# Kernel tuning notes

Measured on AMD Instinct MI355X. Metric: run time of the kernel, lower is better.

The kernel has to match this reference:

```python
import jax, jax.numpy as jnp
import numpy as np
import math
from jax.scipy.special import gammaln

B, H, W = 32, 960, 960
BLOCK = 96  # official NIQE/NRQM block size

# AGGD shape-parameter lookup table (same grid as torch impl: 0.2..10 step 0.001)
_GAM_NP = np.arange(0.2, 10.0 + 1e-6, 0.001, dtype=np.float64)
_RG_NP = np.array([math.exp(2.0 * math.lgamma(2.0 / g) - math.lgamma(1.0 / g) - math.lgamma(3.0 / g)) for g in _GAM_NP], dtype=np.float32)
GAM = jnp.asarray(_GAM_NP.astype(np.float32))
RGAM = jnp.asarray(_RG_NP)

def _gauss_kernel(size, sigma):
    ax = np.arange(size, dtype=np.float64) - (size - 1) / 2.0
    xx, yy = np.meshgrid(ax, ax)
    k = np.exp(-(xx ** 2 + yy ** 2) / (2.0 * sigma ** 2))
    return (k / k.sum()).astype(np.float32)

K7 = jnp.asarray(_gauss_kernel(7, 7.0 / 6.0))[None, None]  # MSCN window
K3 = jnp.asarray(_gauss_kernel(3, 0.5))[None, None]        # pyramid / downsample kernel

def _conv_same(x, k, edge_pad):
    ph = k.shape[-1] // 2
    mode = 'edge' if edge_pad else 'constant'
    x = jnp.pad(x, ((0, 0), (0, 0), (ph, ph), (ph, ph)), mode=mode)
    return jax.lax.conv_general_dilated(x, k, (1, 1), 'VALID', dimension_numbers=('NCHW', 'OIHW', 'NCHW'))

def _normalize(img):
    # MSCN: (img - mu) / (sigma + 1), replicate padding
    mu = _conv_same(img, K7, True)
    sigma = jnp.sqrt(jnp.abs(_conv_same(img * img, K7, True) - mu * mu))
    return (img - mu) / (sigma + 1.0)

def _downsample(img):
    # gaussian blur (3x3, sigma 0.5, zero same-pad) + stride-2 decimation
    return _conv_same(img, K3, False)[:, :, ::2, ::2]

def _aggd(x):
    # x: [b, nb, h, w]; vectorized AGGD parameter estimation over all blocks
    hw = (-2, -1)
    x2 = x * x
    ml = (x < 0).astype(x.dtype)
    mr = (x > 0).astype(x.dtype)
    cl = jnp.maximum(ml.sum(hw), 1.0)
    cr = jnp.maximum(mr.sum(hw), 1.0)
    lstd = jnp.sqrt((x2 * ml).sum(hw) / cl)
    rstd = jnp.sqrt((x2 * mr).sum(hw) / cr)
    gh = lstd / jnp.maximum(rstd, 1e-12)
    rhat = jnp.mean(jnp.abs(x), hw) ** 2 / jnp.maximum(jnp.mean(x2, hw), 1e-12)
    rhn = rhat * (gh ** 3 + 1.0) * (gh + 1.0) / ((gh * gh + 1.0) ** 2)
    idx = jnp.argmin(jnp.abs(RGAM - rhn[..., None]), axis=-1)  # table lookup
    alpha = GAM[idx]
    conv = jnp.exp(0.5 * (gammaln(1.0 / alpha) - gammaln(3.0 / alpha)))
    return alpha, lstd * conv, rstd * conv

def _features(blocks):
    # 18 features per block: AGGD of block + AGGD of 4 shifted products
    alpha, bl, br = _aggd(blocks)
    feats = [alpha, (bl + br) / 2.0]
    for shift in ((0, 1), (1, 0), (1, 1), (1, -1)):
        sb = jnp.roll(blocks, shift, axis=(2, 3))
        a, l, r = _aggd(blocks * sb)
        mean = (r - l) * jnp.exp(gammaln(2.0 / a) - gammaln(1.0 / a))
        feats += [a, mean, l, r]
    return jnp.stack(feats, axis=-1)  # [b, nb, 18]

def _blocks(x, bs):
    b, _, h, w = x.shape
    nh, nw = h // bs, w // bs
    x = x[:, 0].reshape(b, nh, bs, nw, bs).transpose(0, 1, 3, 2, 4)
    return x.reshape(b, nh * nw, bs, bs)

def setup_inputs() -> dict:
    key = jax.random.key(0)
    k1, k2, k3 = jax.random.split(key, 3)
    X = jax.random.uniform(k1, (B, 1, H, W), jnp.float32) * 255.0
    mu_pris = jax.random.normal(k2, (36,), jnp.float32)
    A = jax.random.normal(k3, (36, 36), jnp.float32)
    cov_pris = A @ A.T / 36.0 + jnp.eye(36, dtype=jnp.float32)  # SPD pristine covariance
    return {"X": X, "mu_pris": mu_pris, "cov_pris": cov_pris}

def reference(X, mu_pris, cov_pris):
    feats = []
    img = X
    for scale in (1, 2):
        xn = _normalize(img)
        feats.append(_features(_blocks(xn, BLOCK // scale)))  # [b, 100, 18]
        if scale == 1:
            img = _downsample(img)
    d = jnp.concatenate(feats, axis=-1)  # [b, nb, 36]
    mu_dist = d.mean(axis=1)  # [b, 36]
    c = d - mu_dist[:, None, :]
    cov_dist = jnp.einsum('bnf,bng->bfg', c, c) / (d.shape[1] - 1)
    invcov = jnp.linalg.pinv((cov_pris[None] + cov_dist) / 2.0)
    diff = mu_pris[None] - mu_dist
    q = jnp.einsum('bf,bfg,bg->b', diff, invcov, diff)
    return jnp.sqrt(jnp.maximum(q, 0.0))
```

## Files before the change

### kernel.cpp

```cpp
#include <hip/hip_runtime.h>
#include <hip/hip_fp16.h>
#include <math.h>

#define NTAB 9801
typedef unsigned int uint;
typedef float f2v __attribute__((ext_vector_type(2)));
typedef _Float16 h2v __attribute__((ext_vector_type(2)));

struct WParams { float w1[7]; float wd[3]; };

__device__ inline __half2 u2h2(uint u) { return __builtin_bit_cast(__half2, u); }
__device__ inline float flo(uint u) { return __low2float(u2h2(u)); }
__device__ inline float fhi(uint u) { return __high2float(u2h2(u)); }
__device__ inline uint pkmul(uint a, uint b) { return __builtin_bit_cast(uint, __hmul2(u2h2(a), u2h2(b))); }
__device__ inline uint pack2(float a, float b) {
    return __builtin_bit_cast(uint, __builtin_amdgcn_cvt_pkrtz(a, b));
}
__device__ inline uint algn16(uint hi, uint lo) {
    return (uint)((((unsigned long long)hi << 32) | lo) >> 16);
}
__device__ inline float fdot2f(uint a, uint b, float c) {
    return __builtin_amdgcn_fdot2(__builtin_bit_cast(h2v, a), __builtin_bit_cast(h2v, b), c, false);
}
__device__ inline float rcpf(float x) { return __builtin_amdgcn_rcpf(x); }

template <int S, bool FUSE_DOWN, typename TIN>
__device__ __forceinline__ void mscn_body(int bid, uint* tin,
                                          const TIN* __restrict__ src,
                                          uint* __restrict__ xn_out,
                                          __half* __restrict__ down_out,
                                          const WParams& wp) {
    constexpr int ROW_W = 132, H_OUT = 28, H_IN = H_OUT + 6, RPT = H_OUT / 2;
    constexpr int NTX = (S + 255) / 256, NTY = (S + H_OUT - 1) / H_OUT;

    const int tid = threadIdx.x;
    const int b  = bid / (NTX * NTY);
    const int t2 = bid % (NTX * NTY);
    const int x0 = min((t2 / NTY) * 256, S - 256);
    const int y0 = min((t2 % NTY) * H_OUT, S - H_OUT);

    const float* w1 = wp.w1;
    uint wA[4], wB[4];
    wA[0] = pack2(0.f, w1[0]);   wA[1] = pack2(w1[1], w1[2]);
    wA[2] = pack2(w1[3], w1[4]); wA[3] = pack2(w1[5], w1[6]);
    wB[0] = pack2(w1[0], w1[1]); wB[1] = pack2(w1[2], w1[3]);
    wB[2] = pack2(w1[4], w1[5]); wB[3] = pack2(w1[6], 0.f);

    const TIN* img = src + (size_t)b * S * S;
    const bool interior = (x0 >= 4) && (x0 <= S - 260) && (y0 >= 3) && (y0 <= S - H_IN + 3);

    if constexpr (sizeof(TIN) == 4) {
        if (interior) {
            const float4* base = reinterpret_cast<const float4*>(
                (const float*)img + (size_t)(y0 - 3) * S + (x0 - 4));
            const int f4row = S / 4;
            for (int i = tid; i < 66 * H_IN; i += 256) {
                int r = i / 66, k = i - r * 66;
                float4 v = base[(size_t)r * f4row + k];
                uint2 pr; pr.x = pack2(v.x, v.y); pr.y = pack2(v.z, v.w);
                *(uint2*)&tin[r * ROW_W + 2 * k] = pr;
            }
        } else {
            for (int i = tid; i < ROW_W * H_IN; i += 256) {
                int r = i / ROW_W, w = i - r * ROW_W;
                int gy = y0 + r - 3; gy = gy < 0 ? 0 : (gy >= S ? S - 1 : gy);
                int c0 = x0 - 4 + 2 * w; int c0c = c0 < 0 ? 0 : (c0 >= S ? S - 1 : c0);
                int c1 = c0 + 1;         int c1c = c1 < 0 ? 0 : (c1 >= S ? S - 1 : c1);
                const TIN* rp = img + (size_t)gy * S;
                tin[i] = pack2((float)rp[c0c], (float)rp[c1c]);
            }
        }
    } else {
        const uint* gw = (const uint*)img;
        for (int i = tid; i < ROW_W * H_IN; i += 256) {
            int r = i / ROW_W, w = i - r * ROW_W;
            int gy = y0 + r - 3; gy = gy < 0 ? 0 : (gy >= S ? S - 1 : gy);
            int c0 = x0 - 4 + 2 * w;
            if (c0 >= 0 && c0 + 1 < S) {
                tin[i] = gw[((size_t)gy * S + c0) >> 1];
            } else {
                int c0c = c0 < 0 ? 0 : (c0 >= S ? S - 1 : c0);
                int c1c = (c0 + 1) < 0 ? 0 : ((c0 + 1) >= S ? S - 1 : c0 + 1);
                const TIN* rp = img + (size_t)gy * S;
                tin[i] = pack2((float)rp[c0c], (float)rp[c1c]);
            }
        }
    }
    __syncthreads();

    const int g = tid >> 7, c = tid & 127;
    const int R0 = g * RPT;

    auto horiz = [&](int row, f2v& o1, f2v& o2) {
        const uint* pw = &tin[row * ROW_W + c];
        uint q0 = pw[0], q1 = pw[1], q2 = pw[2], q3 = pw[3], q4 = pw[4];
        uint p0 = pkmul(q0, q0), p1 = pkmul(q1, q1), p2 = pkmul(q2, q2),
             p3 = pkmul(q3, q3), p4 = pkmul(q4, q4);
        float s1A = fdot2f(q3, wA[3], fdot2f(q2, wA[2], fdot2f(q1, wA[1], fdot2f(q0, wA[0], 0.f))));
        float s2A = fdot2f(p3, wA[3], fdot2f(p2, wA[2], fdot2f(p1, wA[1], fdot2f(p0, wA[0], 0.f))));
        float s1B = fdot2f(q4, wB[3], fdot2f(q3, wB[2], fdot2f(q2, wB[1], fdot2f(q1, wB[0], 0.f))));
        float s2B = fdot2f(p4, wB[3], fdot2f(p3, wB[2], fdot2f(p2, wB[1], fdot2f(p1, wB[0], 0.f))));
        o1 = (f2v){s1A, s1B};
        o2 = (f2v){s2A, s2B};
    };

    f2v r1[7], r2[7];
#pragma unroll
    for (int ir = 0; ir < 6; ir++) horiz(R0 + ir, r1[ir], r2[ir]);

    uint* xnp = xn_out + ((((size_t)b * S + y0 + R0) * S + x0) >> 1) + c;
#pragma unroll
    for (int u = 0; u < RPT; u++) {
        horiz(R0 + u + 6, r1[(u + 6) % 7], r2[(u + 6) % 7]);
        f2v a1 = (f2v)(0.f), a2 = (f2v)(0.f);
#pragma unroll
        for (int dy = 0; dy < 7; dy++) {
            a1 += r1[(u + dy) % 7] * w1[dy];
            a2 += r2[(u + dy) % 7] * w1[dy];
        }
        uint qc = tin[(R0 + u + 3) * ROW_W + c + 2];
        float v0a = flo(qc), v0b = fhi(qc);
        float xa = (v0a - a1.x) * rcpf(sqrtf(fabsf(a2.x - a1.x * a1.x)) + 1.f);
        float xb = (v0b - a1.y) * rcpf(sqrtf(fabsf(a2.y - a1.y * a1.y)) + 1.f);
        xnp[(size_t)u * (S / 2)] = pack2(xa, xb);
    }

    if constexpr (FUSE_DOWN) {
        const float* wd = wp.wd;
        const int d = tid & 127, hf = tid >> 7;
        const int Xd = x0 / 2 + d;
        const float mL = (x0 + 2 * d - 1 >= 0) ? 1.f : 0.f;
#pragma unroll
        for (int jj = 0; jj < RPT / 2; jj++) {
            int j = 2 * jj + hf;
            int Yd = y0 / 2 + j;
            float acc = 0.f;
#pragma unroll
            for (int a = 0; a < 3; a++) {
                int gy = 2 * Yd - 1 + a;
                if (gy < 0) continue;
                int tr = gy - y0 + 3;
                uint u1 = tin[tr * ROW_W + d + 1];
                uint u2 = tin[tr * ROW_W + d + 2];
                float rs = wd[0] * fhi(u1) * mL + wd[1] * flo(u2) + wd[2] * fhi(u2);
                acc += wd[a] * rs;
            }
            down_out[((size_t)b * (S / 2) + Yd) * (S / 2) + Xd] = __float2half(acc);
        }
    }
}

template <int BS>
__device__ __forceinline__ void feat2_body(int bid, uint* xs, float* red, float* tot,
                                           const __half* __restrict__ xnimg, int S,
                                           const float* __restrict__ rgam,
                                           const float* __restrict__ gam,
                                           float* __restrict__ dfeat, int foff) {
    constexpr int WROW = BS / 2;
    constexpr int NWORD = BS * BS / 2;
    constexpr int PAIRS = NWORD / 2;
    constexpr int PPR = WROW / 2;

    const int tid = threadIdx.x;
    const int b   = bid / 100;
    const int blk = bid % 100;
    const int by  = (blk / 10) * BS;
    const int bx  = (blk % 10) * BS;

    const uint* gw = (const uint*)xnimg;
    uint4* xs4 = (uint4*)xs;
    constexpr int NW4 = NWORD / 4;
    constexpr int W4R = WROW / 4;
    for (int i = tid; i < NW4; i += 256) {
        int y = i / W4R, k = i - y * W4R;
        xs4[i] = *(const uint4*)&gw[((((size_t)b * S + by + y) * S + bx) >> 1) + 4 * k];
    }
    __syncthreads();

    float ssq[5], sab[5], ssg[5];
    uint  cnt[5];
#pragma unroll
    for (int v = 0; v < 5; v++) { ssq[v] = sab[v] = ssg[v] = 0.f; cnt[v] = 0u; }

    const uint ONE2 = 0x3C003C00u;

    for (int k = 0; k < (PAIRS + 255) / 256; k++) {
        int idx = tid + k * 256;
        if (idx < PAIRS) {
            int y  = idx / PPR;
            int pr = idx - y * PPR;
            int w0 = pr * 2;
            int rb = y * WROW, rbm = (y ? y - 1 : BS - 1) * WROW;
            uint2 V = *(const uint2*)&xs[rb + w0];
            uint WL  = xs[rb  + (w0 ? w0 - 1 : WROW - 1)];
            uint2 A = *(const uint2*)&xs[rbm + w0];
            uint AL  = xs[rbm + (w0 ? w0 - 1 : WROW - 1)];
            uint AR  = xs[rbm + ((w0 + 2 == WROW) ? 0 : w0 + 2)];
            uint vA[5], vB[5];
            vA[0] = V.x;
            vA[1] = pkmul(V.x, algn16(V.x, WL));
            vA[2] = pkmul(V.x, A.x);
            vA[3] = pkmul(V.x, algn16(A.x, AL));
            vA[4] = pkmul(V.x, algn16(A.y, A.x));
            vB[0] = V.y;
            vB[1] = pkmul(V.y, algn16(V.y, V.x));
            vB[2] = pkmul(V.y, A.y);
            vB[3] = pkmul(V.y, algn16(A.y, A.x));
            vB[4] = pkmul(V.y, algn16(AR, A.y));
#pragma unroll
            for (int v = 0; v < 5; v++) {
                uint aA = vA[v] & 0x7FFF7FFFu, aB = vB[v] & 0x7FFF7FFFu;
                ssq[v] = fdot2f(vB[v], vB[v], fdot2f(vA[v], vA[v], ssq[v]));
                sab[v] = fdot2f(aB, ONE2, fdot2f(aA, ONE2, sab[v]));
                ssg[v] = fdot2f(vB[v], aB, fdot2f(vA[v], aA, ssg[v]));
                cnt[v] += ((vA[v] >> 15) & 0x00010001u) + ((vB[v] >> 15) & 0x00010001u);
            }
        }
    }

    const int wid = tid >> 6, lane = tid & 63;
#pragma unroll
    for (int v = 0; v < 5; v++) {
        float a = ssq[v], bb = sab[v], cc = ssg[v];
        float dd = (float)((cnt[v] & 0xFFFFu) + (cnt[v] >> 16));
        for (int off = 32; off >= 1; off >>= 1) {
            a += __shfl_down(a, off); bb += __shfl_down(bb, off);
            cc += __shfl_down(cc, off); dd += __shfl_down(dd, off);
        }
        if (lane == 0) {
            red[wid * 20 + v]      = a;
            red[wid * 20 + 5 + v]  = bb;
            red[wid * 20 + 10 + v] = cc;
            red[wid * 20 + 15 + v] = dd;
        }
    }
    __syncthreads();
    if (tid < 20) tot[tid] = red[tid] + red[20 + tid] + red[40 + tid] + red[60 + tid];
    __syncthreads();

    if (tid < 5) {
        const int v = tid;
        const float N = (float)(BS * BS);
        float ssqv = tot[v], sabv = tot[5 + v], ssgv = tot[10 + v], clv = tot[15 + v];
        float sql = fmaxf(0.5f * (ssqv - ssgv), 0.f);
        float sqr = fmaxf(0.5f * (ssqv + ssgv), 0.f);
        float cl = fmaxf(clv, 1.f), cr = fmaxf(N - clv, 1.f);
        float lstd = sqrtf(sql / cl), rstd = sqrtf(sqr / cr);
        float gh = lstd / fmaxf(rstd, 1e-12f);
        float mabs = sabv / N, msq = ssqv / N;
        float rhat = (mabs * mabs) / fmaxf(msq, 1e-12f);
        float gh2 = gh * gh;
        float target = rhat * (gh * gh2 + 1.f) * (gh + 1.f) / ((gh2 + 1.f) * (gh2 + 1.f));

        int lo = 0, hi = NTAB - 1, j = NTAB;
        while (lo <= hi) {
            int mid = (lo + hi) >> 1;
            if (rgam[mid] >= target) { j = mid; hi = mid - 1; } else lo = mid + 1;
        }
        int i0 = j > 0 ? j - 1 : 0;
        int i1 = j < NTAB ? j : NTAB - 1;
        float d0 = fabsf(rgam[i0] - target);
        float d1 = fabsf(rgam[i1] - target);
        int bi = (d1 < d0) ? i1 : i0;

        float alpha = gam[bi];
        float conv  = expf(0.5f * (lgammaf(1.f / alpha) - lgammaf(3.f / alpha)));
        float bl = lstd * conv, br = rstd * conv;
        float* outp = dfeat + ((size_t)b * 100 + blk) * 36 + foff;
        if (v == 0) {
            outp[0] = alpha;
            outp[1] = 0.5f * (bl + br);
        } else {
            float mean = (br - bl) * expf(lgammaf(2.f / alpha) - lgammaf(1.f / alpha));
            int base = 2 + (v - 1) * 4;
            outp[base + 0] = alpha; outp[base + 1] = mean;
            outp[base + 2] = bl;    outp[base + 3] = br;
        }
    }
}

__global__ __launch_bounds__(256, 8) void mscnA_k(const float* __restrict__ X,
                                                  uint* __restrict__ xn960,
                                                  __half* __restrict__ img480,
                                                  WParams wp,
                                                  float* __restrict__ rgam,
                                                  float* __restrict__ gam) {
    constexpr int NBLK = 32 * 4 * 35;
    if (blockIdx.x >= (unsigned)NBLK) {
        int i = (blockIdx.x - NBLK) * 256 + threadIdx.x;
        if (i < NTAB) {
            double g = 0.2 + (double)i * 0.001;
            double v = exp(2.0 * lgamma(2.0 / g) - lgamma(1.0 / g) - lgamma(3.0 / g));
            rgam[i] = (float)v;
            gam[i]  = (float)g;
        }
        return;
    }
    __shared__ __align__(16) uint tin[132 * 34];
    mscn_body<960, true, float>(blockIdx.x, tin, X, xn960, img480, wp);
}

__global__ __launch_bounds__(256, 8) void launchB_k(const __half* __restrict__ img480,
                                                    uint* __restrict__ xn480,
                                                    const __half* __restrict__ xn960,
                                                    WParams wp,
                                                    const float* __restrict__ rgam,
                                                    const float* __restrict__ gam,
                                                    float* __restrict__ dfeat) {
    constexpr int NB480 = 32 * 2 * 18;
    __shared__ __align__(16) uint smem[4608 + 100];
    if (blockIdx.x < (unsigned)NB480) {
        mscn_body<480, false, __half>(blockIdx.x, smem, img480, xn480, nullptr, wp);
    } else {
        float* red = (float*)(smem + 4608);
        float* tot = red + 80;
        feat2_body<96>(blockIdx.x - NB480, smem, red, tot, xn960, 960, rgam, gam, dfeat, 0);
    }
}

__global__ __launch_bounds__(256, 8) void feat48_k(const __half* __restrict__ xn480,
                                                   const float* __restrict__ rgam,
                                                   const float* __restrict__ gam,
                                                   float* __restrict__ dfeat) {
    __shared__ __align__(16) uint smem[1152 + 100];
    float* red = (float*)(smem + 1152);
    float* tot = red + 80;
    feat2_body<48>(blockIdx.x, smem, red, tot, xn480, 480, rgam, gam, dfeat, 18);
}

__global__ __launch_bounds__(256) void final_k(const float* __restrict__ dfeat,
                                               const float* __restrict__ mu_pris,
                                               const float* __restrict__ cov_pris,
                                               float* __restrict__ out) {
    __shared__ float  ds[3600];
    __shared__ float  mu[36];
    __shared__ double M[36][37];
    __shared__ double rhs[36];
    __shared__ double qacc;
    const int b = blockIdx.x, tid = threadIdx.x;
    const float* src = dfeat + (size_t)b * 3600;
    for (int i = tid; i < 3600; i += 256) ds[i] = src[i];
    __syncthreads();
    if (tid < 36) {
        float s = 0.f;
        for (int n = 0; n < 100; n++) s += ds[n * 36 + tid];
        mu[tid] = s / 100.f;
    }
    __syncthreads();
    for (int i = tid; i < 3600; i += 256) ds[i] -= mu[i % 36];
    if (tid < 36) rhs[tid] = (double)mu_pris[tid] - (double)mu[tid];
    if (tid == 0) qacc = 0.0;
    __syncthreads();
    for (int e = tid; e < 1296; e += 256) {
        int f = e / 36, g = e % 36;
        float s = 0.f;
        for (int n = 0; n < 100; n++) s += ds[n * 36 + f] * ds[n * 36 + g];
        M[f][g] = 0.5 * ((double)cov_pris[e] + (double)(s / 99.f));
    }
    __syncthreads();
    for (int j = 0; j < 36; j++) {
        if (tid == 0) qacc += rhs[j] * rhs[j] / M[j][j];
        int i = j + 1 + tid;
        if (i < 36) {
            double L = M[i][j] / M[j][j];
            for (int k = j; k < 36; k++) M[i][k] -= L * M[j][k];
            rhs[i] -= L * rhs[j];
        }
        __syncthreads();
    }
    if (tid == 0) out[b] = sqrtf((float)(qacc > 0.0 ? qacc : 0.0));
}

static WParams make_weights() {
    WParams p;
    double wt[7], s = 0.0; const double sg = 7.0 / 6.0;
    for (int i = 0; i < 7; i++) { double d = i - 3; wt[i] = exp(-d * d / (2.0 * sg * sg)); s += wt[i]; }
    for (int i = 0; i < 7; i++) p.w1[i] = (float)(wt[i] / s);
    double e1 = exp(-2.0), sd = 1.0 + 2.0 * e1;
    p.wd[0] = p.wd[2] = (float)(e1 / sd);
    p.wd[1] = (float)(1.0 / sd);
    return p;
}

extern "C" void kernel_launch(void* const* d_in, const int* in_sizes, int n_in,
                              void* d_out, int out_size, void* d_ws, size_t ws_size,
                              hipStream_t stream) {
    const float* X        = (const float*)d_in[0];
    const float* mu_pris  = (const float*)d_in[1];
    const float* cov_pris = (const float*)d_in[2];
    float* out = (float*)d_out;

    char* ws = (char*)d_ws;
    float*  rgam   = (float*)(ws);
    float*  gam    = (float*)(ws + 39424);
    float*  dfeat  = (float*)(ws + 78848);
    __half* xn960  = (__half*)(ws + 539648);
    __half* img480 = (__half*)(ws + 59522048);
    __half* xn480  = (__half*)(ws + 74267648);

    WParams wp = make_weights();

    constexpr int NB960 = 32 * 4 * 35;
    constexpr int TBLB  = (NTAB + 255) / 256;
    mscnA_k<<<NB960 + TBLB, 256, 0, stream>>>(X, (uint*)xn960, img480, wp, rgam, gam);
    launchB_k<<<32 * 2 * 18 + 3200, 256, 0, stream>>>(img480, (uint*)xn480, xn960, wp,
                                                      rgam, gam, dfeat);
    feat48_k<<<3200, 256, 0, stream>>>(xn480, rgam, gam, dfeat);
    final_k<<<32, 256, 0, stream>>>(dfeat, mu_pris, cov_pris, out);
}
```

Baseline: 207.1 us.

## Fuse MSCN normalization with per-block feature extraction, dropping normalized-image round trip

Each workgroup now computes MSCN for one 96x96 (or 48x48) feature block directly from a haloed input tile in shared memory and feeds the result straight into feature extraction. This removes the global write and re-read of the full normalized images at both scales. The downsampled image is still written for the second scale. The cost is recomputing halo rows and columns per block, lower occupancy from the larger shared-memory footprint (launch bounds 4), and idle threads during the MSCN stage. The lookup-table build moves into its own small kernel.

```diff
diff --git a/kernel.cpp b/kernel.cpp
--- a/kernel.cpp
+++ b/kernel.cpp
@@ -24,75 +24,31 @@
 }
 __device__ inline float rcpf(float x) { return __builtin_amdgcn_rcpf(x); }
 
-template <int S, bool FUSE_DOWN, typename TIN>
-__device__ __forceinline__ void mscn_body(int bid, uint* tin,
-                                          const TIN* __restrict__ src,
-                                          uint* __restrict__ xn_out,
-                                          __half* __restrict__ down_out,
-                                          const WParams& wp) {
-    constexpr int ROW_W = 132, H_OUT = 28, H_IN = H_OUT + 6, RPT = H_OUT / 2;
-    constexpr int NTX = (S + 255) / 256, NTY = (S + H_OUT - 1) / H_OUT;
-
-    const int tid = threadIdx.x;
-    const int b  = bid / (NTX * NTY);
-    const int t2 = bid % (NTX * NTY);
-    const int x0 = min((t2 / NTY) * 256, S - 256);
-    const int y0 = min((t2 % NTY) * H_OUT, S - H_OUT);
-
-    const float* w1 = wp.w1;
+__global__ __launch_bounds__(256) void tables_k(float* __restrict__ rgam,
+                                                float* __restrict__ gam) {
+    int i = blockIdx.x * 256 + threadIdx.x;
+    if (i >= NTAB) return;
+    double g = 0.2 + (double)i * 0.001;
+    double v = exp(2.0 * lgamma(2.0 / g) - lgamma(1.0 / g) - lgamma(3.0 / g));
+    rgam[i] = (float)v;
+    gam[i]  = (float)g;
+}
+
+template <int CW, int TW, int NG, int RPG, int ORR>
+__device__ __forceinline__ void mscn_tile(const uint* tin, uint* xs,
+                                          const float* w1, int tid) {
+    constexpr int TAIL = ORR - (NG - 1) * RPG;
+    const int g = tid / CW, c = tid - g * CW;
+    const int R0 = g * RPG;
+
     uint wA[4], wB[4];
     wA[0] = pack2(0.f, w1[0]);   wA[1] = pack2(w1[1], w1[2]);
     wA[2] = pack2(w1[3], w1[4]); wA[3] = pack2(w1[5], w1[6]);
     wB[0] = pack2(w1[0], w1[1]); wB[1] = pack2(w1[2], w1[3]);
     wB[2] = pack2(w1[4], w1[5]); wB[3] = pack2(w1[6], 0.f);
 
-    const TIN* img = src + (size_t)b * S * S;
-    const bool interior = (x0 >= 4) && (x0 <= S - 260) && (y0 >= 3) && (y0 <= S - H_IN + 3);
-
-    if constexpr (sizeof(TIN) == 4) {
-        if (interior) {
-            const float4* base = reinterpret_cast<const float4*>(
-                (const float*)img + (size_t)(y0 - 3) * S + (x0 - 4));
-            const int f4row = S / 4;
-            for (int i = tid; i < 66 * H_IN; i += 256) {
-                int r = i / 66, k = i - r * 66;
-                float4 v = base[(size_t)r * f4row + k];
-                uint2 pr; pr.x = pack2(v.x, v.y); pr.y = pack2(v.z, v.w);
-                *(uint2*)&tin[r * ROW_W + 2 * k] = pr;
-            }
-        } else {
-            for (int i = tid; i < ROW_W * H_IN; i += 256) {
-                int r = i / ROW_W, w = i - r * ROW_W;
-                int gy = y0 + r - 3; gy = gy < 0 ? 0 : (gy >= S ? S - 1 : gy);
-                int c0 = x0 - 4 + 2 * w; int c0c = c0 < 0 ? 0 : (c0 >= S ? S - 1 : c0);
-                int c1 = c0 + 1;         int c1c = c1 < 0 ? 0 : (c1 >= S ? S - 1 : c1);
-                const TIN* rp = img + (size_t)gy * S;
-                tin[i] = pack2((float)rp[c0c], (float)rp[c1c]);
-            }
-        }
-    } else {
-        const uint* gw = (const uint*)img;
-        for (int i = tid; i < ROW_W * H_IN; i += 256) {
-            int r = i / ROW_W, w = i - r * ROW_W;
-            int gy = y0 + r - 3; gy = gy < 0 ? 0 : (gy >= S ? S - 1 : gy);
-            int c0 = x0 - 4 + 2 * w;
-            if (c0 >= 0 && c0 + 1 < S) {
-                tin[i] = gw[((size_t)gy * S + c0) >> 1];
-            } else {
-                int c0c = c0 < 0 ? 0 : (c0 >= S ? S - 1 : c0);
-                int c1c = (c0 + 1) < 0 ? 0 : ((c0 + 1) >= S ? S - 1 : c0 + 1);
-                const TIN* rp = img + (size_t)gy * S;
-                tin[i] = pack2((float)rp[c0c], (float)rp[c1c]);
-            }
-        }
-    }
-    __syncthreads();
-
-    const int g = tid >> 7, c = tid & 127;
-    const int R0 = g * RPT;
-
     auto horiz = [&](int row, f2v& o1, f2v& o2) {
-        const uint* pw = &tin[row * ROW_W + c];
+        const uint* pw = &tin[row * TW + c];
         uint q0 = pw[0], q1 = pw[1], q2 = pw[2], q3 = pw[3], q4 = pw[4];
         uint p0 = pkmul(q0, q0), p1 = pkmul(q1, q1), p2 = pkmul(q2, q2),
              p3 = pkmul(q3, q3), p4 = pkmul(q4, q4);
@@ -108,74 +64,43 @@
 #pragma unroll
     for (int ir = 0; ir < 6; ir++) horiz(R0 + ir, r1[ir], r2[ir]);
 
-    uint* xnp = xn_out + ((((size_t)b * S + y0 + R0) * S + x0) >> 1) + c;
-#pragma unroll
-    for (int u = 0; u < RPT; u++) {
-        horiz(R0 + u + 6, r1[(u + 6) % 7], r2[(u + 6) % 7]);
-        f2v a1 = (f2v)(0.f), a2 = (f2v)(0.f);
-#pragma unroll
-        for (int dy = 0; dy < 7; dy++) {
-            a1 += r1[(u + dy) % 7] * w1[dy];
-            a2 += r2[(u + dy) % 7] * w1[dy];
-        }
-        uint qc = tin[(R0 + u + 3) * ROW_W + c + 2];
-        float v0a = flo(qc), v0b = fhi(qc);
-        float xa = (v0a - a1.x) * rcpf(sqrtf(fabsf(a2.x - a1.x * a1.x)) + 1.f);
-        float xb = (v0b - a1.y) * rcpf(sqrtf(fabsf(a2.y - a1.y * a1.y)) + 1.f);
-        xnp[(size_t)u * (S / 2)] = pack2(xa, xb);
-    }
-
-    if constexpr (FUSE_DOWN) {
-        const float* wd = wp.wd;
-        const int d = tid & 127, hf = tid >> 7;
-        const int Xd = x0 / 2 + d;
-        const float mL = (x0 + 2 * d - 1 >= 0) ? 1.f : 0.f;
-#pragma unroll
-        for (int jj = 0; jj < RPT / 2; jj++) {
-            int j = 2 * jj + hf;
-            int Yd = y0 / 2 + j;
-            float acc = 0.f;
-#pragma unroll
-            for (int a = 0; a < 3; a++) {
-                int gy = 2 * Yd - 1 + a;
-                if (gy < 0) continue;
-                int tr = gy - y0 + 3;
-                uint u1 = tin[tr * ROW_W + d + 1];
-                uint u2 = tin[tr * ROW_W + d + 2];
-                float rs = wd[0] * fhi(u1) * mL + wd[1] * flo(u2) + wd[2] * fhi(u2);
-                acc += wd[a] * rs;
-            }
-            down_out[((size_t)b * (S / 2) + Yd) * (S / 2) + Xd] = __float2half(acc);
-        }
-    }
+#define MSCN_STEP(u)                                                          \
+    {                                                                         \
+        horiz(R0 + (u) + 6, r1[((u) + 6) % 7], r2[((u) + 6) % 7]);            \
+        f2v a1 = (f2v)(0.f), a2 = (f2v)(0.f);                                 \
+        _Pragma("unroll")                                                     \
+        for (int dy = 0; dy < 7; dy++) {                                      \
+            a1 += r1[((u) + dy) % 7] * w1[dy];                                \
+            a2 += r2[((u) + dy) % 7] * w1[dy];                                \
+        }                                                                     \
+        uint qc = tin[(R0 + (u) + 3) * TW + c + 2];                           \
+        float v0a = flo(qc), v0b = fhi(qc);                                   \
+        float xa = (v0a - a1.x) * rcpf(sqrtf(fabsf(a2.x - a1.x * a1.x)) + 1.f);\
+        float xb = (v0b - a1.y) * rcpf(sqrtf(fabsf(a2.y - a1.y * a1.y)) + 1.f);\
+        xs[(R0 + (u)) * CW + c] = pack2(xa, xb);                              \
+    }
+
+#pragma unroll
+    for (int u = 0; u < TAIL; u++) MSCN_STEP(u)
+    if constexpr (TAIL < RPG) {
+        if (g < NG - 1) {
+#pragma unroll
+            for (int u = TAIL; u < RPG; u++) MSCN_STEP(u)
+        }
+    }
+#undef MSCN_STEP
 }
 
 template <int BS>
-__device__ __forceinline__ void feat2_body(int bid, uint* xs, float* red, float* tot,
-                                           const __half* __restrict__ xnimg, int S,
-                                           const float* __restrict__ rgam,
-                                           const float* __restrict__ gam,
-                                           float* __restrict__ dfeat, int foff) {
+__device__ __forceinline__ void feat_core(const uint* xs, float* red, float* tot,
+                                          int b, int blk,
+                                          const float* __restrict__ rgam,
+                                          const float* __restrict__ gam,
+                                          float* __restrict__ dfeat, int foff) {
     constexpr int WROW = BS / 2;
-    constexpr int NWORD = BS * BS / 2;
-    constexpr int PAIRS = NWORD / 2;
+    constexpr int PAIRS = BS * BS / 4;
     constexpr int PPR = WROW / 2;
-
     const int tid = threadIdx.x;
-    const int b   = bid / 100;
-    const int blk = bid % 100;
-    const int by  = (blk / 10) * BS;
-    const int bx  = (blk % 10) * BS;
-
-    const uint* gw = (const uint*)xnimg;
-    uint4* xs4 = (uint4*)xs;
-    constexpr int NW4 = NWORD / 4;
-    constexpr int W4R = WROW / 4;
-    for (int i = tid; i < NW4; i += 256) {
-        int y = i / W4R, k = i - y * W4R;
-        xs4[i] = *(const uint4*)&gw[((((size_t)b * S + by + y) * S + bx) >> 1) + 4 * k];
-    }
-    __syncthreads();
 
     float ssq[5], sab[5], ssg[5];
     uint  cnt[5];
@@ -279,53 +204,116 @@
     }
 }
 
-__global__ __launch_bounds__(256, 8) void mscnA_k(const float* __restrict__ X,
-                                                  uint* __restrict__ xn960,
-                                                  __half* __restrict__ img480,
-                                                  WParams wp,
-                                                  float* __restrict__ rgam,
-                                                  float* __restrict__ gam) {
-    constexpr int NBLK = 32 * 4 * 35;
-    if (blockIdx.x >= (unsigned)NBLK) {
-        int i = (blockIdx.x - NBLK) * 256 + threadIdx.x;
-        if (i < NTAB) {
-            double g = 0.2 + (double)i * 0.001;
-            double v = exp(2.0 * lgamma(2.0 / g) - lgamma(1.0 / g) - lgamma(3.0 / g));
-            rgam[i] = (float)v;
-            gam[i]  = (float)g;
-        }
-        return;
-    }
-    __shared__ __align__(16) uint tin[132 * 34];
-    mscn_body<960, true, float>(blockIdx.x, tin, X, xn960, img480, wp);
-}
-
-__global__ __launch_bounds__(256, 8) void launchB_k(const __half* __restrict__ img480,
-                                                    uint* __restrict__ xn480,
-                                                    const __half* __restrict__ xn960,
-                                                    WParams wp,
-                                                    const float* __restrict__ rgam,
-                                                    const float* __restrict__ gam,
-                                                    float* __restrict__ dfeat) {
-    constexpr int NB480 = 32 * 2 * 18;
-    __shared__ __align__(16) uint smem[4608 + 100];
-    if (blockIdx.x < (unsigned)NB480) {
-        mscn_body<480, false, __half>(blockIdx.x, smem, img480, xn480, nullptr, wp);
+__global__ __launch_bounds__(256, 4) void fused960_k(const float* __restrict__ X,
+                                                     __half* __restrict__ img480,
+                                                     const float* __restrict__ rgam,
+                                                     const float* __restrict__ gam,
+                                                     float* __restrict__ dfeat,
+                                                     WParams wp) {
+    __shared__ __align__(16) uint tin[52 * 102];
+    __shared__ __align__(16) uint xs[48 * 96];
+    __shared__ float red[80];
+    __shared__ float tot[20];
+
+    const int tid = threadIdx.x;
+    const int b   = blockIdx.x / 100;
+    const int blk = blockIdx.x % 100;
+    const int br  = blk / 10, bc = blk % 10;
+    const int by  = br * 96, bx = bc * 96;
+
+    const float* img = X + (size_t)b * 960 * 960;
+    const bool interior = (br >= 1) && (br <= 8) && (bc >= 1) && (bc <= 8);
+
+    if (interior) {
+        const float4* base = reinterpret_cast<const float4*>(
+            img + (size_t)(by - 3) * 960 + (bx - 4));
+        for (int i = tid; i < 26 * 102; i += 256) {
+            int r = i / 26, k = i - r * 26;
+            float4 v = base[(size_t)r * 240 + k];
+            tin[r * 52 + 2 * k]     = pack2(v.x, v.y);
+            tin[r * 52 + 2 * k + 1] = pack2(v.z, v.w);
+        }
     } else {
-        float* red = (float*)(smem + 4608);
-        float* tot = red + 80;
-        feat2_body<96>(blockIdx.x - NB480, smem, red, tot, xn960, 960, rgam, gam, dfeat, 0);
-    }
-}
-
-__global__ __launch_bounds__(256, 8) void feat48_k(const __half* __restrict__ xn480,
-                                                   const float* __restrict__ rgam,
-                                                   const float* __restrict__ gam,
-                                                   float* __restrict__ dfeat) {
-    __shared__ __align__(16) uint smem[1152 + 100];
-    float* red = (float*)(smem + 1152);
-    float* tot = red + 80;
-    feat2_body<48>(blockIdx.x, smem, red, tot, xn480, 480, rgam, gam, dfeat, 18);
+        for (int i = tid; i < 52 * 102; i += 256) {
+            int r = i / 52, w = i - r * 52;
+            int gy = by + r - 3; gy = gy < 0 ? 0 : (gy > 959 ? 959 : gy);
+            int c0 = bx - 4 + 2 * w; int c0c = c0 < 0 ? 0 : (c0 > 959 ? 959 : c0);
+            int c1 = c0 + 1;         int c1c = c1 < 0 ? 0 : (c1 > 959 ? 959 : c1);
+            const float* rp = img + (size_t)gy * 960;
+            tin[i] = pack2(rp[c0c], rp[c1c]);
+        }
+    }
+    __syncthreads();
+
+    if (tid < 240) mscn_tile<48, 52, 5, 20, 96>(tin, xs, wp.w1, tid);
+
+    {
+        const float* wd = wp.wd;
+#pragma unroll
+        for (int k = 0; k < 9; k++) {
+            int o = tid + k * 256;
+            int j = o / 48, d = o - j * 48;
+            int Yd = by / 2 + j, Xd = bx / 2 + d;
+            float mL = (bx + 2 * d - 1 >= 0) ? 1.f : 0.f;
+            float acc = 0.f;
+#pragma unroll
+            for (int a = 0; a < 3; a++) {
+                int gy = 2 * Yd - 1 + a;
+                if (gy < 0) continue;
+                int tr = gy - by + 3;
+                uint u1 = tin[tr * 52 + d + 1];
+                uint u2 = tin[tr * 52 + d + 2];
+                acc += wd[a] * (wd[0] * fhi(u1) * mL + wd[1] * flo(u2) + wd[2] * fhi(u2));
+            }
+            img480[((size_t)b * 480 + Yd) * 480 + Xd] = __float2half(acc);
+        }
+    }
+    __syncthreads();
+
+    feat_core<96>(xs, red, tot, b, blk, rgam, gam, dfeat, 0);
+}
+
+__global__ __launch_bounds__(256, 8) void fused480_k(const __half* __restrict__ img480,
+                                                     const float* __restrict__ rgam,
+                                                     const float* __restrict__ gam,
+                                                     float* __restrict__ dfeat,
+                                                     WParams wp) {
+    __shared__ __align__(16) uint tin[28 * 54];
+    __shared__ __align__(16) uint xs[24 * 48];
+    __shared__ float red[80];
+    __shared__ float tot[20];
+
+    const int tid = threadIdx.x;
+    const int b   = blockIdx.x / 100;
+    const int blk = blockIdx.x % 100;
+    const int br  = blk / 10, bc = blk % 10;
+    const int by  = br * 48, bx = bc * 48;
+
+    const __half* img = img480 + (size_t)b * 480 * 480;
+    const uint* gw = (const uint*)img;
+    const bool interior = (br >= 1) && (br <= 8) && (bc >= 1) && (bc <= 8);
+
+    if (interior) {
+        for (int i = tid; i < 28 * 54; i += 256) {
+            int r = i / 28, w = i - r * 28;
+            tin[i] = gw[(((size_t)(by + r - 3) * 480 + (bx - 4)) >> 1) + w];
+        }
+    } else {
+        for (int i = tid; i < 28 * 54; i += 256) {
+            int r = i / 28, w = i - r * 28;
+            int gy = by + r - 3; gy = gy < 0 ? 0 : (gy > 479 ? 479 : gy);
+            int c0 = bx - 4 + 2 * w; int c0c = c0 < 0 ? 0 : (c0 > 479 ? 479 : c0);
+            int c1 = c0 + 1;         int c1c = c1 < 0 ? 0 : (c1 > 479 ? 479 : c1);
+            const __half* rp = img + (size_t)gy * 480;
+            tin[i] = pack2(__half2float(rp[c0c]), __half2float(rp[c1c]));
+        }
+    }
+    __syncthreads();
+
+    if (tid < 192) mscn_tile<24, 28, 8, 6, 48>(tin, xs, wp.w1, tid);
+    __syncthreads();
+
+    feat_core<48>(xs, red, tot, b, blk, rgam, gam, dfeat, 18);
 }
 
 __global__ __launch_bounds__(256) void final_k(const float* __restrict__ dfeat,
@@ -394,17 +382,12 @@
     float*  rgam   = (float*)(ws);
     float*  gam    = (float*)(ws + 39424);
     float*  dfeat  = (float*)(ws + 78848);
-    __half* xn960  = (__half*)(ws + 539648);
-    __half* img480 = (__half*)(ws + 59522048);
-    __half* xn480  = (__half*)(ws + 74267648);
+    __half* img480 = (__half*)(ws + 539648);
 
     WParams wp = make_weights();
 
-    constexpr int NB960 = 32 * 4 * 35;
-    constexpr int TBLB  = (NTAB + 255) / 256;
-    mscnA_k<<<NB960 + TBLB, 256, 0, stream>>>(X, (uint*)xn960, img480, wp, rgam, gam);
-    launchB_k<<<32 * 2 * 18 + 3200, 256, 0, stream>>>(img480, (uint*)xn480, xn960, wp,
-                                                      rgam, gam, dfeat);
-    feat48_k<<<3200, 256, 0, stream>>>(xn480, rgam, gam, dfeat);
+    tables_k<<<(NTAB + 255) / 256, 256, 0, stream>>>(rgam, gam);
+    fused960_k<<<3200, 256, 0, stream>>>(X, img480, rgam, gam, dfeat, wp);
+    fused480_k<<<3200, 256, 0, stream>>>(img480, rgam, gam, dfeat, wp);
     final_k<<<32, 256, 0, stream>>>(dfeat, mu_pris, cov_pris, out);
 }
```

Result: faster. 199.1 us (-3.8%).
